# Kernel optimization log

Measured on AMD Instinct MI355X. Metric: run time of the kernel, lower is better.

## Reference

```python
import jax, jax.numpy as jnp
import numpy as np
import math

L, B, E, H = 1024, 4, 1024, 16
HD = E // H

def setup_inputs() -> dict:
    key = jax.random.key(0)
    ks = jax.random.split(key, 8)
    bound_in = math.sqrt(6.0 / (3 * E + E))  # xavier_uniform for [3E, E]
    bound_out = math.sqrt(1.0 / E)           # default Linear init
    return {
        "query": jax.random.normal(ks[0], (L, B, E), jnp.float32),
        "key": jax.random.normal(ks[1], (L, B, E), jnp.float32),
        "value": jax.random.normal(ks[2], (L, B, E), jnp.float32),
        "attn_mask": jnp.zeros((B, L, L), jnp.float32),
        "in_proj_weight": jax.random.uniform(ks[3], (3 * E, E), jnp.float32, -bound_in, bound_in),
        "in_proj_bias": jnp.zeros((3 * E,), jnp.float32),
        "out_proj_weight": jax.random.uniform(ks[4], (E, E), jnp.float32, -bound_out, bound_out),
        "out_proj_bias": jnp.zeros((E,), jnp.float32),
    }

def reference(query, key, value, attn_mask, in_proj_weight, in_proj_bias,
              out_proj_weight, out_proj_bias):
    # packed in-projection: q/k/v [L, B, E]
    q = query @ in_proj_weight[:E].T + in_proj_bias[:E]
    k = key @ in_proj_weight[E:2 * E].T + in_proj_bias[E:2 * E]
    v = value @ in_proj_weight[2 * E:].T + in_proj_bias[2 * E:]
    # [L, B, E] -> [B*H, L, HD]
    def to_heads(x):
        return x.reshape(L, B * H, HD).transpose(1, 0, 2)
    qh, kh, vh = to_heads(q), to_heads(k), to_heads(v)
    qh = qh / math.sqrt(HD)
    scores = jnp.einsum('bqd,bkd->bqk', qh, kh)  # [B*H, L, L]
    # per-batch mask repeated across heads: [B,L,L] -> [B*H,L,L]
    mask = jnp.repeat(attn_mask, H, axis=0)
    weights = jax.nn.softmax(scores + mask, axis=-1)
    out = jnp.einsum('bqk,bkd->bqd', weights, vh)  # [B*H, L, HD]
    out = out.transpose(1, 0, 2).reshape(L, B, E)
    attn_output = out @ out_proj_weight.T + out_proj_bias
    avg_weights = weights.reshape(B, H, L, L).mean(axis=1)
    return attn_output, avg_weights
```

## Files before the change

### kernel.cpp

```cpp
#include <hip/hip_runtime.h>
#include <hip/hip_bf16.h>
#include <cstdint>
#include <cstddef>

#define LL 1024
#define BB 4
#define EE 1024
#define HH 16
#define HD 64
#define NHEADS 64

typedef __bf16 bf16x8 __attribute__((ext_vector_type(8)));
typedef float f32x4 __attribute__((ext_vector_type(4)));
typedef unsigned short u16;
typedef unsigned char u8;

__device__ __forceinline__ u16 f2b(float f) {
  union { float f; unsigned int i; } v; v.f = f;
  unsigned int r = v.i + 0x7FFFu + ((v.i >> 16) & 1u);
  return (u16)(r >> 16);
}
__device__ __forceinline__ float fp8d(u8 b) {
  return __builtin_amdgcn_cvt_f32_fp8((int)b, 0);
}

__device__ __forceinline__ void gload16(const u16* g, u16* l) {
  __builtin_amdgcn_global_load_lds(
      (const __attribute__((address_space(1))) unsigned int*)(const void*)g,
      (__attribute__((address_space(3))) unsigned int*)(void*)l, 16, 0, 0);
}

#define CVT_TOTAL 5242880
__global__ __launch_bounds__(256)
void cvt_all(const float* __restrict__ q, const float* __restrict__ k,
             const float* __restrict__ v, const float* __restrict__ wi,
             const float* __restrict__ wo, const float* __restrict__ mask,
             u16* __restrict__ qb, u16* __restrict__ kb, u16* __restrict__ vb,
             u16* __restrict__ wib, u16* __restrict__ wob,
             unsigned int* __restrict__ emask) {
  int i = blockIdx.x * 256 + threadIdx.x;
  if (i >= CVT_TOTAL) return;
  if (i >= 4194304) {
    int off = i - 4194304;
    const float4 t = ((const float4*)mask)[off];
    int lo = __builtin_amdgcn_cvt_pk_fp8_f32(__expf(t.x), __expf(t.y), 0, false);
    int vv = __builtin_amdgcn_cvt_pk_fp8_f32(__expf(t.z), __expf(t.w), lo, true);
    emask[off] = (unsigned int)vv;
    return;
  }
  const float* s; u16* d; int off;
  if (i < 1048576)      { s = q;  d = qb;  off = i; }
  else if (i < 2097152) { s = k;  d = kb;  off = i - 1048576; }
  else if (i < 3145728) { s = v;  d = vb;  off = i - 2097152; }
  else if (i < 3932160) { s = wi; d = wib; off = i - 3145728; }
  else                  { s = wo; d = wob; off = i - 3932160; }
  const float4 t = ((const float4*)s)[off];
  u16 o[4] = { f2b(t.x), f2b(t.y), f2b(t.z), f2b(t.w) };
  *(uint2*)&d[(size_t)off * 4] = *(const uint2*)o;
}

__global__ __launch_bounds__(256, 3)
void gemm_in(const u16* __restrict__ A0, const u16* __restrict__ A1,
             const u16* __restrict__ A2, const u16* __restrict__ Bw,
             const float* __restrict__ bias,
             u16* __restrict__ Oq, u16* __restrict__ Ok, u16* __restrict__ Ov) {
  const int tid  = threadIdx.x;
  const int lane = tid & 63;
  const int wave = tid >> 6;
  const int quad = lane >> 4;
  const int l15  = lane & 15;
  const int wm = wave >> 1, wn = wave & 1;
  const int row0 = blockIdx.x * 128;
  const int col0 = blockIdx.y * 128;
  const int K = EE;

  const int sec = col0 >> 10;
  const u16* A = (sec == 0) ? A0 : ((sec == 1) ? A1 : A2);

  __shared__ __align__(16) u16 lA[2][4][128][8];
  __shared__ __align__(16) u16 lB[2][4][128][8];

  f32x4 acc[4][4];
#pragma unroll
  for (int i = 0; i < 4; ++i)
#pragma unroll
    for (int j = 0; j < 4; ++j) { acc[i][j][0]=0.f; acc[i][j][1]=0.f; acc[i][j][2]=0.f; acc[i][j][3]=0.f; }

#pragma unroll
  for (int p = 0; p < 2; ++p) {
    int lc = p * 256 + tid;
    int r = lc & 127, g = lc >> 7;
    gload16(A  + (size_t)(row0 + r) * K + (g << 3), &lA[0][0][0][0] + lc * 8);
    gload16(Bw + (size_t)(col0 + r) * K + (g << 3), &lB[0][0][0][0] + lc * 8);
  }

  int buf = 0;
  for (int k0 = 0; k0 < K; k0 += 32) {
    __syncthreads();
    if (k0 + 32 < K) {
#pragma unroll
      for (int p = 0; p < 2; ++p) {
        int lc = p * 256 + tid;
        int r = lc & 127, g = lc >> 7;
        gload16(A  + (size_t)(row0 + r) * K + (k0 + 32 + (g << 3)), &lA[buf ^ 1][0][0][0] + lc * 8);
        gload16(Bw + (size_t)(col0 + r) * K + (k0 + 32 + (g << 3)), &lB[buf ^ 1][0][0][0] + lc * 8);
      }
    }
    bf16x8 af[4], bfr[4];
#pragma unroll
    for (int i = 0; i < 4; ++i) af[i]  = *(const bf16x8*)&lA[buf][quad][wm * 64 + i * 16 + l15][0];
#pragma unroll
    for (int j = 0; j < 4; ++j) bfr[j] = *(const bf16x8*)&lB[buf][quad][wn * 64 + j * 16 + l15][0];
#pragma unroll
    for (int i = 0; i < 4; ++i)
#pragma unroll
      for (int j = 0; j < 4; ++j)
        acc[i][j] = __builtin_amdgcn_mfma_f32_16x16x32_bf16(af[i], bfr[j], acc[i][j], 0, 0, 0);
    buf ^= 1;
  }

#pragma unroll
  for (int i = 0; i < 4; ++i) {
    const int grb = row0 + wm * 64 + i * 16 + quad * 4;
#pragma unroll
    for (int j = 0; j < 4; ++j) {
      const int gc = col0 + wn * 64 + j * 16 + l15;
      const float bv = bias[gc];
#pragma unroll
      for (int r = 0; r < 4; ++r) {
        float val = acc[i][j][r] + bv;
        const int gr = grb + r;
        const int l = gr >> 2, b = gr & 3;
        const int e = gc & 1023;
        const int h = e >> 6, d = e & 63;
        const int n = b * 16 + h;
        if (sec == 0)      Oq[((size_t)n * LL + l) * HD + d] = f2b(val * 0.125f);
        else if (sec == 1) Ok[((size_t)n * LL + l) * HD + d] = f2b(val);
        else               Ov[((size_t)n * HD + d) * LL + l] = f2b(val);
      }
    }
  }
}

__global__ __launch_bounds__(256, 2)
void gemm_out(const u16* __restrict__ A, const u16* __restrict__ Bw,
              const float* __restrict__ bias, float* __restrict__ Of) {
  const int tid  = threadIdx.x;
  const int lane = tid & 63;
  const int wave = tid >> 6;
  const int quad = lane >> 4;
  const int l15  = lane & 15;
  const int wm = wave >> 1, wn = wave & 1;
  const int row0 = blockIdx.x * 64;
  const int col0 = blockIdx.y * 128;
  const int K = EE;

  __shared__ __align__(16) u16 lA[2][4][64][8];
  __shared__ __align__(16) u16 lB[2][4][128][8];

  f32x4 acc[2][4];
#pragma unroll
  for (int i = 0; i < 2; ++i)
#pragma unroll
    for (int j = 0; j < 4; ++j) { acc[i][j][0]=0.f; acc[i][j][1]=0.f; acc[i][j][2]=0.f; acc[i][j][3]=0.f; }

  {
    int r = tid & 63, g = tid >> 6;
    gload16(A + (size_t)(row0 + r) * K + (g << 3), &lA[0][0][0][0] + tid * 8);
#pragma unroll
    for (int p = 0; p < 2; ++p) {
      int lc = p * 256 + tid;
      int rb = lc & 127, gb = lc >> 7;
      gload16(Bw + (size_t)(col0 + rb) * K + (gb << 3), &lB[0][0][0][0] + lc * 8);
    }
  }

  int buf = 0;
  for (int k0 = 0; k0 < K; k0 += 32) {
    __syncthreads();
    if (k0 + 32 < K) {
      int r = tid & 63, g = tid >> 6;
      gload16(A + (size_t)(row0 + r) * K + (k0 + 32 + (g << 3)), &lA[buf ^ 1][0][0][0] + tid * 8);
#pragma unroll
      for (int p = 0; p < 2; ++p) {
        int lc = p * 256 + tid;
        int rb = lc & 127, gb = lc >> 7;
        gload16(Bw + (size_t)(col0 + rb) * K + (k0 + 32 + (gb << 3)), &lB[buf ^ 1][0][0][0] + lc * 8);
      }
    }
    bf16x8 af[2], bfr[4];
#pragma unroll
    for (int i = 0; i < 2; ++i) af[i]  = *(const bf16x8*)&lA[buf][quad][wm * 32 + i * 16 + l15][0];
#pragma unroll
    for (int j = 0; j < 4; ++j) bfr[j] = *(const bf16x8*)&lB[buf][quad][wn * 64 + j * 16 + l15][0];
#pragma unroll
    for (int i = 0; i < 2; ++i)
#pragma unroll
      for (int j = 0; j < 4; ++j)
        acc[i][j] = __builtin_amdgcn_mfma_f32_16x16x32_bf16(af[i], bfr[j], acc[i][j], 0, 0, 0);
    buf ^= 1;
  }

#pragma unroll
  for (int i = 0; i < 2; ++i) {
    const int grb = row0 + wm * 32 + i * 16 + quad * 4;
#pragma unroll
    for (int j = 0; j < 4; ++j) {
      const int gc = col0 + wn * 64 + j * 16 + l15;
      const float bv = bias[gc];
#pragma unroll
      for (int r = 0; r < 4; ++r)
        Of[(size_t)(grb + r) * EE + gc] = acc[i][j][r] + bv;
    }
  }
}

__global__ __launch_bounds__(256, 2)
void attn_fused(const u16* __restrict__ Qh, const u16* __restrict__ Kh,
                const u16* __restrict__ Vt, const u8* __restrict__ emask,
                float* __restrict__ rsbuf, u16* __restrict__ O) {
  const int tid = threadIdx.x, lane = tid & 63, wave = tid >> 6;
  const int quad = lane >> 4, l15 = lane & 15;
  const int n = blockIdx.x;
  const int q0 = blockIdx.y * 128;
  const int b = n >> 4, h = n & 15;
  const int qw = wave * 32;

  __shared__ __align__(16) u16 lQ[8][128][8];
  __shared__ __align__(16) u16 lK[2][8][64][8];
  __shared__ __align__(16) u16 lV[2][8][64][8];
  __shared__ __align__(16) u16 lW[128][72];

  const u16* Qb = Qh + ((size_t)n * LL + q0) * HD;
  const u16* Kb = Kh + (size_t)n * LL * HD;
  const u16* Vb = Vt + (size_t)n * HD * LL;

#pragma unroll
  for (int p = 0; p < 4; ++p) {
    int lc = p * 256 + tid;
    gload16(Qb + (lc & 127) * HD + ((lc >> 7) << 3), &lQ[0][0][0] + lc * 8);
  }
#pragma unroll
  for (int p = 0; p < 2; ++p) {
    int lc = p * 256 + tid;
    gload16(Kb + (size_t)(lc & 63) * HD + ((lc >> 6) << 3), &lK[0][0][0][0] + lc * 8);
    gload16(Vb + (size_t)(lc & 63) * LL + ((lc >> 6) << 3),  &lV[0][0][0][0] + lc * 8);
  }
  __syncthreads();

  bf16x8 aq[2][2];
#pragma unroll
  for (int jq = 0; jq < 2; ++jq) {
    aq[jq][0] = *(const bf16x8*)&lQ[quad][qw + jq * 16 + l15][0];
    aq[jq][1] = *(const bf16x8*)&lQ[4 + quad][qw + jq * 16 + l15][0];
  }

  float sr[8] = {0.f,0.f,0.f,0.f,0.f,0.f,0.f,0.f};
  f32x4 ctx[2][4];
#pragma unroll
  for (int jq = 0; jq < 2; ++jq)
#pragma unroll
    for (int j = 0; j < 4; ++j) { ctx[jq][j][0]=0.f; ctx[jq][j][1]=0.f; ctx[jq][j][2]=0.f; ctx[jq][j][3]=0.f; }

  int buf = 0;
  for (int kc = 0; kc < 16; ++kc) {
    if (kc < 15) {
#pragma unroll
      for (int p = 0; p < 2; ++p) {
        int lc = p * 256 + tid;
        gload16(Kb + (size_t)((kc + 1) * 64 + (lc & 63)) * HD + ((lc >> 6) << 3),
                &lK[buf ^ 1][0][0][0] + lc * 8);
        gload16(Vb + (size_t)(lc & 63) * LL + (kc + 1) * 64 + ((lc >> 6) << 3),
                &lV[buf ^ 1][0][0][0] + lc * 8);
      }
    }

#pragma unroll
    for (int jq = 0; jq < 2; ++jq) {
      f32x4 sc[4];
#pragma unroll
      for (int jk = 0; jk < 4; ++jk) {
        bf16x8 bk0 = *(const bf16x8*)&lK[buf][quad][jk * 16 + l15][0];
        bf16x8 bk1 = *(const bf16x8*)&lK[buf][4 + quad][jk * 16 + l15][0];
        f32x4 a; a[0]=0.f; a[1]=0.f; a[2]=0.f; a[3]=0.f;
        a = __builtin_amdgcn_mfma_f32_16x16x32_bf16(aq[jq][0], bk0, a, 0, 0, 0);
        a = __builtin_amdgcn_mfma_f32_16x16x32_bf16(aq[jq][1], bk1, a, 0, 0, 0);
        sc[jk] = a;
      }
#pragma unroll
      for (int r = 0; r < 4; ++r) {
        const int q = q0 + qw + jq * 16 + quad * 4 + r;
        const u8* mp = emask + ((size_t)b << 20) + (size_t)q * LL + kc * 64 + l15;
        float ss = 0.0f;
#pragma unroll
        for (int jk = 0; jk < 4; ++jk) {
          float w = fp8d(mp[jk * 16]) * __expf(sc[jk][r]);
          ss += w;
          lW[qw + jq * 16 + quad * 4 + r][jk * 16 + l15] = f2b(w);
        }
        sr[jq * 4 + r] += ss;
      }
    }

#pragma unroll
    for (int jq = 0; jq < 2; ++jq)
#pragma unroll
      for (int ks = 0; ks < 2; ++ks) {
        bf16x8 aw = *(const bf16x8*)&lW[qw + jq * 16 + l15][ks * 32 + quad * 8];
#pragma unroll
        for (int j = 0; j < 4; ++j) {
          bf16x8 bv = *(const bf16x8*)&lV[buf][ks * 4 + quad][j * 16 + l15][0];
          ctx[jq][j] = __builtin_amdgcn_mfma_f32_16x16x32_bf16(aw, bv, ctx[jq][j], 0, 0, 0);
        }
      }

    __syncthreads();
    buf ^= 1;
  }

  float rs[8];
#pragma unroll
  for (int i = 0; i < 8; ++i) {
#pragma unroll
    for (int d = 1; d < 16; d <<= 1) sr[i] += __shfl_xor(sr[i], d);
    rs[i] = 1.0f / sr[i];
  }
#pragma unroll
  for (int jq = 0; jq < 2; ++jq)
#pragma unroll
    for (int j = 0; j < 4; ++j) {
      const int d = j * 16 + l15;
#pragma unroll
      for (int r = 0; r < 4; ++r) {
        const int l = q0 + qw + jq * 16 + quad * 4 + r;
        O[((size_t)l * BB + b) * EE + h * 64 + d] = f2b(ctx[jq][j][r] * rs[jq * 4 + r]);
      }
    }
  if (l15 == 0) {
#pragma unroll
    for (int jq = 0; jq < 2; ++jq)
#pragma unroll
      for (int r = 0; r < 4; ++r) {
        const int q = q0 + qw + jq * 16 + quad * 4 + r;
        rsbuf[n * LL + q] = rs[jq * 4 + r];
      }
  }
}

__global__ __launch_bounds__(256, 2)
void attn_avg(const u16* __restrict__ Qh, const u16* __restrict__ Kh,
              const u8* __restrict__ emask, const float* __restrict__ rsbuf,
              float* __restrict__ avgout) {
  const int tid = threadIdx.x, lane = tid & 63, wave = tid >> 6;
  const int quad = lane >> 4, l15 = lane & 15;
  const int kc = blockIdx.x;
  const int q0 = blockIdx.y * 64;
  const int b = blockIdx.z;

  __shared__ __align__(16) u16 lQ[2][8][64][8];
  __shared__ __align__(16) u16 lK[2][8][128][8];

  float acc[8][4];
#pragma unroll
  for (int j = 0; j < 8; ++j)
#pragma unroll
    for (int r = 0; r < 4; ++r) acc[j][r] = 0.0f;

  const int qrb = q0 + wave * 16;

  {
    const int n0 = b * 16;
    const u16* Qb = Qh + ((size_t)n0 * LL + q0) * HD;
    const u16* Kb = Kh + ((size_t)n0 * LL + kc * 128) * HD;
#pragma unroll
    for (int p = 0; p < 2; ++p) {
      int lc = p * 256 + tid;
      gload16(Qb + (lc & 63) * HD + ((lc >> 6) << 3), &lQ[0][0][0][0] + lc * 8);
    }
#pragma unroll
    for (int p = 0; p < 4; ++p) {
      int lc = p * 256 + tid;
      gload16(Kb + (size_t)(lc & 127) * HD + ((lc >> 7) << 3), &lK[0][0][0][0] + lc * 8);
    }
  }

  for (int h = 0; h < 16; ++h) {
    const int buf = h & 1;
    __syncthreads();
    if (h < 15) {
      const int n1 = b * 16 + h + 1;
      const u16* Qb = Qh + ((size_t)n1 * LL + q0) * HD;
      const u16* Kb = Kh + ((size_t)n1 * LL + kc * 128) * HD;
#pragma unroll
      for (int p = 0; p < 2; ++p) {
        int lc = p * 256 + tid;
        gload16(Qb + (lc & 63) * HD + ((lc >> 6) << 3), &lQ[buf ^ 1][0][0][0] + lc * 8);
      }
#pragma unroll
      for (int p = 0; p < 4; ++p) {
        int lc = p * 256 + tid;
        gload16(Kb + (size_t)(lc & 127) * HD + ((lc >> 7) << 3), &lK[buf ^ 1][0][0][0] + lc * 8);
      }
    }

    const int n = b * 16 + h;
    float rs[4];
#pragma unroll
    for (int r = 0; r < 4; ++r) {
      const int q = qrb + quad * 4 + r;
      rs[r] = rsbuf[n * LL + q];
    }
    bf16x8 aq0 = *(const bf16x8*)&lQ[buf][quad][wave * 16 + l15][0];
    bf16x8 aq1 = *(const bf16x8*)&lQ[buf][4 + quad][wave * 16 + l15][0];
#pragma unroll
    for (int j = 0; j < 8; ++j) {
      bf16x8 bk0 = *(const bf16x8*)&lK[buf][quad][j * 16 + l15][0];
      bf16x8 bk1 = *(const bf16x8*)&lK[buf][4 + quad][j * 16 + l15][0];
      f32x4 a; a[0]=0.f; a[1]=0.f; a[2]=0.f; a[3]=0.f;
      a = __builtin_amdgcn_mfma_f32_16x16x32_bf16(aq0, bk0, a, 0, 0, 0);
      a = __builtin_amdgcn_mfma_f32_16x16x32_bf16(aq1, bk1, a, 0, 0, 0);
#pragma unroll
      for (int r = 0; r < 4; ++r) acc[j][r] += __expf(a[r]) * rs[r];
    }
  }
#pragma unroll
  for (int j = 0; j < 8; ++j) {
#pragma unroll
    for (int r = 0; r < 4; ++r) {
      const int q = qrb + quad * 4 + r;
      const int k = kc * 128 + j * 16 + l15;
      const size_t idx = ((size_t)b << 20) + (size_t)q * LL + k;
      avgout[idx] = acc[j][r] * 0.0625f * fp8d(emask[idx]);
    }
  }
}

extern "C" void kernel_launch(void* const* d_in, const int* in_sizes, int n_in,
                              void* d_out, int out_size, void* d_ws, size_t ws_size,
                              hipStream_t stream) {
  const float* query = (const float*)d_in[0];
  const float* key   = (const float*)d_in[1];
  const float* value = (const float*)d_in[2];
  const float* mask  = (const float*)d_in[3];
  const float* win   = (const float*)d_in[4];
  const float* bin   = (const float*)d_in[5];
  const float* wout  = (const float*)d_in[6];
  const float* bout  = (const float*)d_in[7];
  float* out = (float*)d_out;

  u16* qb    = (u16*)d_ws;
  u16* kb    = qb + (size_t)LL * BB * EE;
  u16* vb    = kb + (size_t)LL * BB * EE;
  u16* winb  = vb + (size_t)LL * BB * EE;
  u16* woutb = winb + (size_t)3 * EE * EE;
  u16* Qh = woutb + (size_t)EE * EE;
  u16* Kh = Qh + (size_t)NHEADS * LL * HD;
  u16* Vt = Kh + (size_t)NHEADS * LL * HD;
  u16* O  = Vt + (size_t)NHEADS * LL * HD;
  float* rsbuf = (float*)(O + (size_t)LL * BB * EE);
  u8* emask = (u8*)(rsbuf + NHEADS * LL);

  dim3 blk(256);
  cvt_all<<<dim3((CVT_TOTAL + 255) / 256), blk, 0, stream>>>(
      query, key, value, win, wout, mask, qb, kb, vb, winb, woutb,
      (unsigned int*)emask);
  gemm_in<<<dim3(32, 24), blk, 0, stream>>>(qb, kb, vb, winb, bin, Qh, Kh, Vt);
  attn_fused<<<dim3(64, 8), blk, 0, stream>>>(Qh, Kh, Vt, emask, rsbuf, O);
  attn_avg<<<dim3(8, 16, 4), blk, 0, stream>>>(Qh, Kh, emask, rsbuf, out + (size_t)LL * BB * EE);
  gemm_out<<<dim3(64, 8), blk, 0, stream>>>(O, woutb, bout, out);
}
```

Baseline: 299.9 us.

## Triple-buffer LDS staging in projection GEMMs with partial vmcnt waits

Both projection GEMMs move from a double-buffered LDS pipeline with a full __syncthreads per k-step to a three-stage ring buffer. Each step waits only until the oldest outstanding global-to-LDS load has landed (s_waitcnt vmcnt(N)), then issues the load two steps ahead before computing. The goal is to hide global load latency behind MFMA work. In exchange it uses more LDS, which may lower occupancy, and correctness depends on the hand-set vmcnt counts matching the number of loads each stage issues.

```diff
diff --git a/kernel.cpp b/kernel.cpp
--- a/kernel.cpp
+++ b/kernel.cpp
@@ -72,13 +72,12 @@
   const int wm = wave >> 1, wn = wave & 1;
   const int row0 = blockIdx.x * 128;
   const int col0 = blockIdx.y * 128;
-  const int K = EE;
 
   const int sec = col0 >> 10;
   const u16* A = (sec == 0) ? A0 : ((sec == 1) ? A1 : A2);
 
-  __shared__ __align__(16) u16 lA[2][4][128][8];
-  __shared__ __align__(16) u16 lB[2][4][128][8];
+  __shared__ __align__(16) u16 lA[3][4][128][8];
+  __shared__ __align__(16) u16 lB[3][4][128][8];
 
   f32x4 acc[4][4];
 #pragma unroll
@@ -86,38 +85,43 @@
 #pragma unroll
     for (int j = 0; j < 4; ++j) { acc[i][j][0]=0.f; acc[i][j][1]=0.f; acc[i][j][2]=0.f; acc[i][j][3]=0.f; }
 
-#pragma unroll
-  for (int p = 0; p < 2; ++p) {
-    int lc = p * 256 + tid;
-    int r = lc & 127, g = lc >> 7;
-    gload16(A  + (size_t)(row0 + r) * K + (g << 3), &lA[0][0][0][0] + lc * 8);
-    gload16(Bw + (size_t)(col0 + r) * K + (g << 3), &lB[0][0][0][0] + lc * 8);
-  }
-
-  int buf = 0;
-  for (int k0 = 0; k0 < K; k0 += 32) {
-    __syncthreads();
-    if (k0 + 32 < K) {
-#pragma unroll
-      for (int p = 0; p < 2; ++p) {
-        int lc = p * 256 + tid;
-        int r = lc & 127, g = lc >> 7;
-        gload16(A  + (size_t)(row0 + r) * K + (k0 + 32 + (g << 3)), &lA[buf ^ 1][0][0][0] + lc * 8);
-        gload16(Bw + (size_t)(col0 + r) * K + (k0 + 32 + (g << 3)), &lB[buf ^ 1][0][0][0] + lc * 8);
-      }
-    }
+  auto stage = [&](int k0, int sbuf) {
+#pragma unroll
+    for (int p = 0; p < 2; ++p) {
+      int lc = p * 256 + tid;
+      int r = lc & 127, g = lc >> 7;
+      gload16(A  + (size_t)(row0 + r) * EE + (k0 + (g << 3)), &lA[sbuf][0][0][0] + lc * 8);
+      gload16(Bw + (size_t)(col0 + r) * EE + (k0 + (g << 3)), &lB[sbuf][0][0][0] + lc * 8);
+    }
+  };
+
+  auto compute = [&](int cbuf) {
     bf16x8 af[4], bfr[4];
 #pragma unroll
-    for (int i = 0; i < 4; ++i) af[i]  = *(const bf16x8*)&lA[buf][quad][wm * 64 + i * 16 + l15][0];
-#pragma unroll
-    for (int j = 0; j < 4; ++j) bfr[j] = *(const bf16x8*)&lB[buf][quad][wn * 64 + j * 16 + l15][0];
+    for (int i = 0; i < 4; ++i) af[i]  = *(const bf16x8*)&lA[cbuf][quad][wm * 64 + i * 16 + l15][0];
+#pragma unroll
+    for (int j = 0; j < 4; ++j) bfr[j] = *(const bf16x8*)&lB[cbuf][quad][wn * 64 + j * 16 + l15][0];
 #pragma unroll
     for (int i = 0; i < 4; ++i)
 #pragma unroll
       for (int j = 0; j < 4; ++j)
         acc[i][j] = __builtin_amdgcn_mfma_f32_16x16x32_bf16(af[i], bfr[j], acc[i][j], 0, 0, 0);
-    buf ^= 1;
-  }
+  };
+
+  stage(0, 0);
+  stage(32, 1);
+
+  for (int it = 0; it < 31; ++it) {
+    asm volatile("s_waitcnt vmcnt(4)" ::: "memory");
+    __builtin_amdgcn_s_barrier();
+    __builtin_amdgcn_sched_barrier(0);
+    if (it < 30) stage((it + 2) * 32, (it + 2) % 3);
+    compute(it % 3);
+  }
+  asm volatile("s_waitcnt vmcnt(0)" ::: "memory");
+  __builtin_amdgcn_s_barrier();
+  __builtin_amdgcn_sched_barrier(0);
+  compute(31 % 3);
 
 #pragma unroll
   for (int i = 0; i < 4; ++i) {
@@ -153,10 +157,9 @@
   const int wm = wave >> 1, wn = wave & 1;
   const int row0 = blockIdx.x * 64;
   const int col0 = blockIdx.y * 128;
-  const int K = EE;
-
-  __shared__ __align__(16) u16 lA[2][4][64][8];
-  __shared__ __align__(16) u16 lB[2][4][128][8];
+
+  __shared__ __align__(16) u16 lA[3][4][64][8];
+  __shared__ __align__(16) u16 lB[3][4][128][8];
 
   f32x4 acc[2][4];
 #pragma unroll
@@ -164,42 +167,44 @@
 #pragma unroll
     for (int j = 0; j < 4; ++j) { acc[i][j][0]=0.f; acc[i][j][1]=0.f; acc[i][j][2]=0.f; acc[i][j][3]=0.f; }
 
-  {
+  auto stage = [&](int k0, int sbuf) {
     int r = tid & 63, g = tid >> 6;
-    gload16(A + (size_t)(row0 + r) * K + (g << 3), &lA[0][0][0][0] + tid * 8);
+    gload16(A + (size_t)(row0 + r) * EE + (k0 + (g << 3)), &lA[sbuf][0][0][0] + tid * 8);
 #pragma unroll
     for (int p = 0; p < 2; ++p) {
       int lc = p * 256 + tid;
       int rb = lc & 127, gb = lc >> 7;
-      gload16(Bw + (size_t)(col0 + rb) * K + (gb << 3), &lB[0][0][0][0] + lc * 8);
-    }
-  }
-
-  int buf = 0;
-  for (int k0 = 0; k0 < K; k0 += 32) {
-    __syncthreads();
-    if (k0 + 32 < K) {
-      int r = tid & 63, g = tid >> 6;
-      gload16(A + (size_t)(row0 + r) * K + (k0 + 32 + (g << 3)), &lA[buf ^ 1][0][0][0] + tid * 8);
-#pragma unroll
-      for (int p = 0; p < 2; ++p) {
-        int lc = p * 256 + tid;
-        int rb = lc & 127, gb = lc >> 7;
-        gload16(Bw + (size_t)(col0 + rb) * K + (k0 + 32 + (gb << 3)), &lB[buf ^ 1][0][0][0] + lc * 8);
-      }
-    }
+      gload16(Bw + (size_t)(col0 + rb) * EE + (k0 + (gb << 3)), &lB[sbuf][0][0][0] + lc * 8);
+    }
+  };
+
+  auto compute = [&](int cbuf) {
     bf16x8 af[2], bfr[4];
 #pragma unroll
-    for (int i = 0; i < 2; ++i) af[i]  = *(const bf16x8*)&lA[buf][quad][wm * 32 + i * 16 + l15][0];
-#pragma unroll
-    for (int j = 0; j < 4; ++j) bfr[j] = *(const bf16x8*)&lB[buf][quad][wn * 64 + j * 16 + l15][0];
+    for (int i = 0; i < 2; ++i) af[i]  = *(const bf16x8*)&lA[cbuf][quad][wm * 32 + i * 16 + l15][0];
+#pragma unroll
+    for (int j = 0; j < 4; ++j) bfr[j] = *(const bf16x8*)&lB[cbuf][quad][wn * 64 + j * 16 + l15][0];
 #pragma unroll
     for (int i = 0; i < 2; ++i)
 #pragma unroll
       for (int j = 0; j < 4; ++j)
         acc[i][j] = __builtin_amdgcn_mfma_f32_16x16x32_bf16(af[i], bfr[j], acc[i][j], 0, 0, 0);
-    buf ^= 1;
-  }
+  };
+
+  stage(0, 0);
+  stage(32, 1);
+
+  for (int it = 0; it < 31; ++it) {
+    asm volatile("s_waitcnt vmcnt(3)" ::: "memory");
+    __builtin_amdgcn_s_barrier();
+    __builtin_amdgcn_sched_barrier(0);
+    if (it < 30) stage((it + 2) * 32, (it + 2) % 3);
+    compute(it % 3);
+  }
+  asm volatile("s_waitcnt vmcnt(0)" ::: "memory");
+  __builtin_amdgcn_s_barrier();
+  __builtin_amdgcn_sched_barrier(0);
+  compute(31 % 3);
 
 #pragma unroll
   for (int i = 0; i < 2; ++i) {
```

New measurement: 301.4 us. Within noise of the previous version (+0.5%).
